# Kernel optimization log

Measured on AMD Instinct MI355X. Metric: run time of the kernel, lower is better.

Reference implementation:

```python
import jax, jax.numpy as jnp
import numpy as np

N, F, V, E = 16384, 39, 100000, 16
H1, H2 = 400, 400
EPS = 1e-5  # BatchNorm eps; eval mode with running_mean=0, running_var=1


def setup_inputs() -> dict:
    key = jax.random.key(0)
    ks = jax.random.split(key, 12)
    Xi = jax.random.randint(ks[0], (N, F, 1), 0, V, dtype=jnp.int32)
    Xv = jax.random.uniform(ks[1], (N, F, 1), dtype=jnp.float32)
    emb1 = jax.random.normal(ks[2], (F, V, 1), dtype=jnp.float32)   # per-field first-order tables
    emb2 = jax.random.normal(ks[3], (F, V, E), dtype=jnp.float32)   # per-field second-order tables
    W1 = jax.random.normal(ks[4], (F * E, H1), dtype=jnp.float32) * (1.0 / np.sqrt(F * E))
    b1 = jnp.zeros((H1,), dtype=jnp.float32)
    W2 = jax.random.normal(ks[5], (H1, H2), dtype=jnp.float32) * (1.0 / np.sqrt(H1))
    b2 = jnp.zeros((H2,), dtype=jnp.float32)
    g1 = jnp.ones((H1,), dtype=jnp.float32)
    beta1 = jnp.zeros((H1,), dtype=jnp.float32)
    g2 = jnp.ones((H2,), dtype=jnp.float32)
    beta2 = jnp.zeros((H2,), dtype=jnp.float32)
    bias = jax.random.normal(ks[6], (1,), dtype=jnp.float32)
    return dict(Xi=Xi, Xv=Xv, emb1=emb1, emb2=emb2, W1=W1, b1=b1, W2=W2, b2=b2,
                g1=g1, beta1=beta1, g2=g2, beta2=beta2, bias=bias)


def reference(Xi, Xv, emb1, emb2, W1, b1, W2, b2, g1, beta1, g2, beta2, bias):
    idx = Xi[:, :, 0]                     # [N, F]
    f_ar = jnp.arange(F)[None, :]         # broadcast field index
    # first order: row-sum of the original [N,N] broadcast equals e1 * sum_b(Xv)
    e1 = emb1[f_ar, idx, 0]               # [N, F]
    first = jnp.sum(e1 * jnp.sum(Xv[:, :, 0], axis=0)[None, :], axis=1)  # [N]
    # second order (FM)
    e2 = emb2[f_ar, idx] * Xv             # [N, F, E]
    s = jnp.sum(e2, axis=1)               # [N, E]
    second = 0.5 * (s * s - jnp.sum(e2 * e2, axis=1))  # [N, E]
    # deep part (BN in eval mode: running_mean=0, running_var=1; dropout off)
    bn_scale = 1.0 / jnp.sqrt(1.0 + EPS)
    h = e2.reshape(e2.shape[0], F * E)
    h = (h @ W1 + b1) * bn_scale * g1 + beta1
    h = (h @ W2 + b2) * bn_scale * g2 + beta2
    return first + jnp.sum(second, axis=1) + jnp.sum(h, axis=1) + bias  # [N]
```

## Files before the change

### kernel.cpp

```cpp
#include <hip/hip_runtime.h>
#include <cstddef>

#define N_SAMPLES 16384
#define F_ 39
#define V_ 100000
#define E_ 16
#define H1_ 400
#define H2_ 400
#define FE_ (F_ * E_)

__device__ __forceinline__ float blockReduceSum256(float v, float* red) {
  int t = threadIdx.x;
  v += __shfl_xor(v, 32);
  v += __shfl_xor(v, 16);
  v += __shfl_xor(v, 8);
  v += __shfl_xor(v, 4);
  v += __shfl_xor(v, 2);
  v += __shfl_xor(v, 1);
  if ((t & 63) == 0) red[t >> 6] = v;
  __syncthreads();
  if (t == 0) v = red[0] + red[1] + red[2] + red[3];
  return v;
}

__global__ __launch_bounds__(256) void pre1_kernel(
    const float* __restrict__ Xv, const float* __restrict__ W2,
    const float* __restrict__ g2, float* __restrict__ colsum,
    float* __restrict__ w2red) {
  __shared__ float red[4];
  int b = blockIdx.x, t = threadIdx.x;
  if (b < F_) {
    float acc = 0.f;
    for (int n = t; n < N_SAMPLES; n += 256) acc += Xv[(size_t)n * F_ + b];
    float tot = blockReduceSum256(acc, red);
    if (t == 0) colsum[b] = tot;
  } else {
    int k = b - F_;
    float acc = 0.f;
    for (int j = t; j < H2_; j += 256) acc += W2[k * H2_ + j] * g2[j];
    float tot = blockReduceSum256(acc, red);
    if (t == 0) w2red[k] = tot;
  }
}

__global__ __launch_bounds__(256) void pre2_kernel(
    const float* __restrict__ W1, const float* __restrict__ b1,
    const float* __restrict__ g1, const float* __restrict__ beta1,
    const float* __restrict__ b2, const float* __restrict__ g2,
    const float* __restrict__ beta2, const float* __restrict__ w2red,
    float* __restrict__ A, float* __restrict__ consts) {
  __shared__ float red[4];
  const float c = 1.0f / sqrtf(1.0f + 1e-5f);
  int b = blockIdx.x, t = threadIdx.x;
  if (b < FE_) {
    float acc = 0.f;
    for (int k = t; k < H1_; k += 256) acc += W1[b * H1_ + k] * g1[k] * w2red[k];
    float tot = blockReduceSum256(acc, red);
    if (t == 0) A[b] = c * c * tot;
  } else {
    float acc = 0.f;
    for (int k = t; k < H1_; k += 256) {
      float wr = w2red[k];
      acc += c * c * b1[k] * g1[k] * wr + c * beta1[k] * wr;
    }
    for (int j = t; j < H2_; j += 256) acc += c * g2[j] * b2[j] + beta2[j];
    float tot = blockReduceSum256(acc, red);
    if (t == 0) consts[0] = tot;
  }
}

__global__ __launch_bounds__(256) void fused_main(
    const int* __restrict__ Xi, const float* __restrict__ Xv,
    const float* __restrict__ emb1, const float* __restrict__ emb2,
    const float* __restrict__ colsum, const float* __restrict__ A,
    const float* __restrict__ consts, const float* __restrict__ bias,
    float* __restrict__ out) {
  __shared__ int s_ix[16][F_ + 1];
  __shared__ float s_xv[16][F_ + 1];
  __shared__ float s_A[FE_];
  __shared__ float s_cs[F_];
  int t = threadIdx.x;
  int n0 = blockIdx.x * 16;

  for (int i = t; i < FE_; i += 256) s_A[i] = A[i];
  if (t < F_) s_cs[t] = colsum[t];
  for (int i = t; i < 16 * F_; i += 256) {
    int smp = i / F_, f = i - smp * F_;
    s_ix[smp][f] = Xi[(n0 + smp) * F_ + f];
    s_xv[smp][f] = Xv[(n0 + smp) * F_ + f];
  }
  __syncthreads();

  int g = t >> 4;
  int j = t & 15;
  float s = 0.f, sq = 0.f, lin = 0.f, first = 0.f;

#pragma unroll
  for (int f = 0; f < F_; ++f) {
    int ix = s_ix[g][f];
    float v = s_xv[g][f];
    float x = emb2[((size_t)(f * V_ + ix)) * E_ + j] * v;
    s += x;
    sq += x * x;
    lin += x * s_A[f * E_ + j];
  }

  for (int f = j; f < F_; f += E_) {
    first += emb1[(size_t)f * V_ + s_ix[g][f]] * s_cs[f];
  }

  float tv = 0.5f * (s * s - sq) + lin + first;
  tv += __shfl_xor(tv, 1);
  tv += __shfl_xor(tv, 2);
  tv += __shfl_xor(tv, 4);
  tv += __shfl_xor(tv, 8);

  if (j == 0) out[n0 + g] = tv + consts[0] + bias[0];
}

extern "C" void kernel_launch(void* const* d_in, const int* in_sizes, int n_in,
                              void* d_out, int out_size, void* d_ws, size_t ws_size,
                              hipStream_t stream) {
  const int* Xi = (const int*)d_in[0];
  const float* Xv = (const float*)d_in[1];
  const float* emb1 = (const float*)d_in[2];
  const float* emb2 = (const float*)d_in[3];
  const float* W1 = (const float*)d_in[4];
  const float* b1 = (const float*)d_in[5];
  const float* W2 = (const float*)d_in[6];
  const float* b2 = (const float*)d_in[7];
  const float* g1 = (const float*)d_in[8];
  const float* beta1 = (const float*)d_in[9];
  const float* g2 = (const float*)d_in[10];
  const float* beta2 = (const float*)d_in[11];
  const float* bias = (const float*)d_in[12];
  float* out = (float*)d_out;

  float* ws = (float*)d_ws;
  float* colsum = ws;
  float* w2red = ws + 64;
  float* A = ws + 512;
  float* consts = ws + 1152;

  pre1_kernel<<<F_ + H1_, 256, 0, stream>>>(Xv, W2, g2, colsum, w2red);
  pre2_kernel<<<FE_ + 1, 256, 0, stream>>>(W1, b1, g1, beta1, b2, g2, beta2,
                                           w2red, A, consts);
  fused_main<<<N_SAMPLES / 16, 256, 0, stream>>>(Xi, Xv, emb1, emb2, colsum, A,
                                                 consts, bias, out);
}
```

Baseline: 371.9 us.

## Parallelize column sums, vectorize weight reductions, use float4 embedding gathers

The column sum of Xv now runs as a two-stage reduction: 256 blocks accumulate into shared-memory bins with atomics, and a later pass combines the partials. Before, 39 blocks each made strided passes over the whole input. The W2·g2 and W1·(g1·w2red) reductions switch to float4 loads, with g1·w2red folded into a precomputed vector. The main kernel now handles 8 samples per block with 32 lanes per sample, and each lane gathers a float4 slice of the embedding row, giving wider memory transactions and more blocks. The cost is extra shuffle reductions, shared-memory atomic contention in the column sum, and an extra workspace buffer.

```diff
diff --git a/kernel.cpp b/kernel.cpp
--- a/kernel.cpp
+++ b/kernel.cpp
@@ -8,6 +8,10 @@
 #define H1_ 400
 #define H2_ 400
 #define FE_ (F_ * E_)
+
+#define CS_BLOCKS 256
+#define CS_CHUNK (N_SAMPLES / CS_BLOCKS)
+#define SPB 8
 
 __device__ __forceinline__ float blockReduceSum256(float v, float* red) {
   int t = threadIdx.x;
@@ -25,21 +29,35 @@
 
 __global__ __launch_bounds__(256) void pre1_kernel(
     const float* __restrict__ Xv, const float* __restrict__ W2,
-    const float* __restrict__ g2, float* __restrict__ colsum,
-    float* __restrict__ w2red) {
-  __shared__ float red[4];
+    const float* __restrict__ g1, const float* __restrict__ g2,
+    float* __restrict__ partial, float* __restrict__ w2red,
+    float* __restrict__ w2g) {
   int b = blockIdx.x, t = threadIdx.x;
-  if (b < F_) {
+  if (b < CS_BLOCKS) {
+    __shared__ float bins[F_];
+    if (t < F_) bins[t] = 0.f;
+    __syncthreads();
+    const float* src = Xv + (size_t)b * CS_CHUNK * F_;
+    for (int i = t; i < CS_CHUNK * F_; i += 256) {
+      int f = i % F_;
+      atomicAdd(&bins[f], src[i]);
+    }
+    __syncthreads();
+    if (t < F_) partial[b * F_ + t] = bins[t];
+  } else {
+    __shared__ float red[4];
+    int k = b - CS_BLOCKS;
     float acc = 0.f;
-    for (int n = t; n < N_SAMPLES; n += 256) acc += Xv[(size_t)n * F_ + b];
-    float tot = blockReduceSum256(acc, red);
-    if (t == 0) colsum[b] = tot;
-  } else {
-    int k = b - F_;
-    float acc = 0.f;
-    for (int j = t; j < H2_; j += 256) acc += W2[k * H2_ + j] * g2[j];
-    float tot = blockReduceSum256(acc, red);
-    if (t == 0) w2red[k] = tot;
+    if (t < H2_ / 4) {
+      const float4 w = reinterpret_cast<const float4*>(W2 + (size_t)k * H2_)[t];
+      const float4 gg = reinterpret_cast<const float4*>(g2)[t];
+      acc = w.x * gg.x + w.y * gg.y + w.z * gg.z + w.w * gg.w;
+    }
+    float tot = blockReduceSum256(acc, red);
+    if (t == 0) {
+      w2red[k] = tot;
+      w2g[k] = tot * g1[k];
+    }
   }
 }
 
@@ -48,16 +66,22 @@
     const float* __restrict__ g1, const float* __restrict__ beta1,
     const float* __restrict__ b2, const float* __restrict__ g2,
     const float* __restrict__ beta2, const float* __restrict__ w2red,
-    float* __restrict__ A, float* __restrict__ consts) {
+    const float* __restrict__ w2g, const float* __restrict__ partial,
+    float* __restrict__ A, float* __restrict__ colsum,
+    float* __restrict__ consts) {
   __shared__ float red[4];
   const float c = 1.0f / sqrtf(1.0f + 1e-5f);
   int b = blockIdx.x, t = threadIdx.x;
   if (b < FE_) {
     float acc = 0.f;
-    for (int k = t; k < H1_; k += 256) acc += W1[b * H1_ + k] * g1[k] * w2red[k];
+    if (t < H1_ / 4) {
+      const float4 w = reinterpret_cast<const float4*>(W1 + (size_t)b * H1_)[t];
+      const float4 gg = reinterpret_cast<const float4*>(w2g)[t];
+      acc = w.x * gg.x + w.y * gg.y + w.z * gg.z + w.w * gg.w;
+    }
     float tot = blockReduceSum256(acc, red);
     if (t == 0) A[b] = c * c * tot;
-  } else {
+  } else if (b == FE_) {
     float acc = 0.f;
     for (int k = t; k < H1_; k += 256) {
       float wr = w2red[k];
@@ -66,61 +90,86 @@
     for (int j = t; j < H2_; j += 256) acc += c * g2[j] * b2[j] + beta2[j];
     float tot = blockReduceSum256(acc, red);
     if (t == 0) consts[0] = tot;
-  }
-}
-
-__global__ __launch_bounds__(256) void fused_main(
+  } else {
+    int f = b - FE_ - 1;
+    float acc = (t < CS_BLOCKS) ? partial[t * F_ + f] : 0.f;
+    float tot = blockReduceSum256(acc, red);
+    if (t == 0) colsum[f] = tot;
+  }
+}
+
+__global__ __launch_bounds__(256, 8) void fused_main(
     const int* __restrict__ Xi, const float* __restrict__ Xv,
     const float* __restrict__ emb1, const float* __restrict__ emb2,
     const float* __restrict__ colsum, const float* __restrict__ A,
     const float* __restrict__ consts, const float* __restrict__ bias,
     float* __restrict__ out) {
-  __shared__ int s_ix[16][F_ + 1];
-  __shared__ float s_xv[16][F_ + 1];
-  __shared__ float s_A[FE_];
+  __shared__ int s_ix[SPB][F_ + 1];
+  __shared__ float s_xv[SPB][F_ + 1];
+  __shared__ __align__(16) float s_A[FE_];
   __shared__ float s_cs[F_];
   int t = threadIdx.x;
-  int n0 = blockIdx.x * 16;
+  int n0 = blockIdx.x * SPB;
 
   for (int i = t; i < FE_; i += 256) s_A[i] = A[i];
   if (t < F_) s_cs[t] = colsum[t];
-  for (int i = t; i < 16 * F_; i += 256) {
+  for (int i = t; i < SPB * F_; i += 256) {
     int smp = i / F_, f = i - smp * F_;
     s_ix[smp][f] = Xi[(n0 + smp) * F_ + f];
     s_xv[smp][f] = Xv[(n0 + smp) * F_ + f];
   }
   __syncthreads();
 
-  int g = t >> 4;
-  int j = t & 15;
-  float s = 0.f, sq = 0.f, lin = 0.f, first = 0.f;
+  int g = t >> 5;
+  int l = t & 31;
+  int q = l & 3;
+  int fs = l >> 2;
+
+  float4 s4 = make_float4(0.f, 0.f, 0.f, 0.f);
+  float sq = 0.f, lin = 0.f, first = 0.f;
 
 #pragma unroll
-  for (int f = 0; f < F_; ++f) {
-    int ix = s_ix[g][f];
-    float v = s_xv[g][f];
-    float x = emb2[((size_t)(f * V_ + ix)) * E_ + j] * v;
-    s += x;
-    sq += x * x;
-    lin += x * s_A[f * E_ + j];
-  }
-
-  for (int f = j; f < F_; f += E_) {
+  for (int i = 0; i < 5; ++i) {
+    int f = fs + 8 * i;
+    if (f < F_) {
+      int ix = s_ix[g][f];
+      float v = s_xv[g][f];
+      const float4 e = *reinterpret_cast<const float4*>(
+          emb2 + ((size_t)(f * V_ + ix)) * E_ + 4 * q);
+      float xx = e.x * v, xy = e.y * v, xz = e.z * v, xw = e.w * v;
+      s4.x += xx; s4.y += xy; s4.z += xz; s4.w += xw;
+      sq += xx * xx + xy * xy + xz * xz + xw * xw;
+      const float4 a = *reinterpret_cast<const float4*>(&s_A[f * E_ + 4 * q]);
+      lin += xx * a.x + xy * a.y + xz * a.z + xw * a.w;
+    }
+  }
+
+  for (int f = l; f < F_; f += 32) {
     first += emb1[(size_t)f * V_ + s_ix[g][f]] * s_cs[f];
   }
 
-  float tv = 0.5f * (s * s - sq) + lin + first;
+  s4.x += __shfl_xor(s4.x, 4);  s4.y += __shfl_xor(s4.y, 4);
+  s4.z += __shfl_xor(s4.z, 4);  s4.w += __shfl_xor(s4.w, 4);
+  s4.x += __shfl_xor(s4.x, 8);  s4.y += __shfl_xor(s4.y, 8);
+  s4.z += __shfl_xor(s4.z, 8);  s4.w += __shfl_xor(s4.w, 8);
+  s4.x += __shfl_xor(s4.x, 16); s4.y += __shfl_xor(s4.y, 16);
+  s4.z += __shfl_xor(s4.z, 16); s4.w += __shfl_xor(s4.w, 16);
+
+  float ss = s4.x * s4.x + s4.y * s4.y + s4.z * s4.z + s4.w * s4.w;
+  float tv = (fs == 0 ? 0.5f * ss : 0.f) - 0.5f * sq + lin + first;
+
   tv += __shfl_xor(tv, 1);
   tv += __shfl_xor(tv, 2);
   tv += __shfl_xor(tv, 4);
   tv += __shfl_xor(tv, 8);
-
-  if (j == 0) out[n0 + g] = tv + consts[0] + bias[0];
+  tv += __shfl_xor(tv, 16);
+
+  if (l == 0) out[n0 + g] = tv + consts[0] + bias[0];
 }
 
 extern "C" void kernel_launch(void* const* d_in, const int* in_sizes, int n_in,
-                              void* d_out, int out_size, void* d_ws, size_t ws_size,
-                              hipStream_t stream) {
+                              void* d_out, int out_size, void* d_ws,
+                              size_t ws_size, hipStream_t stream) {
   const int* Xi = (const int*)d_in[0];
   const float* Xv = (const float*)d_in[1];
   const float* emb1 = (const float*)d_in[2];
@@ -139,12 +188,16 @@
   float* ws = (float*)d_ws;
   float* colsum = ws;
   float* w2red = ws + 64;
-  float* A = ws + 512;
-  float* consts = ws + 1152;
-
-  pre1_kernel<<<F_ + H1_, 256, 0, stream>>>(Xv, W2, g2, colsum, w2red);
-  pre2_kernel<<<FE_ + 1, 256, 0, stream>>>(W1, b1, g1, beta1, b2, g2, beta2,
-                                           w2red, A, consts);
-  fused_main<<<N_SAMPLES / 16, 256, 0, stream>>>(Xi, Xv, emb1, emb2, colsum, A,
-                                                 consts, bias, out);
-}
+  float* w2g = ws + 512;
+  float* A = ws + 960;
+  float* consts = ws + 1600;
+  float* partial = ws + 2048;
+
+  pre1_kernel<<<CS_BLOCKS + H1_, 256, 0, stream>>>(Xv, W2, g1, g2, partial,
+                                                   w2red, w2g);
+  pre2_kernel<<<FE_ + 1 + F_, 256, 0, stream>>>(W1, b1, g1, beta1, b2, g2,
+                                                beta2, w2red, w2g, partial, A,
+                                                colsum, consts);
+  fused_main<<<N_SAMPLES / SPB, 256, 0, stream>>>(Xi, Xv, emb1, emb2, colsum,
+                                                  A, consts, bias, out);
+}
```

New measurement: 345.2 us. -7.2%, faster.
